# Optimization experiments

Measured on AMD Instinct MI355X. Metric: run time of the kernel, lower is better.

Reference implementation:

```python
import jax, jax.numpy as jnp
import numpy as np

N = 100_000      # nodes
E = 1_600_000    # edges
F_IN = 32        # node features
F_E = 8          # edge features
H = 64           # hidden channels
L = 2            # GAT layers
NEG_SLOPE = 0.2


def setup_inputs() -> dict:
    key = jax.random.key(0)
    ks = jax.random.split(key, 20)
    s = 0.05
    return {
        "x": jax.random.normal(ks[0], (N, F_IN), jnp.float32),
        "edge_index": jax.random.randint(ks[1], (2, E), 0, N, jnp.int64),
        "edge_attr": jax.random.normal(ks[2], (E, F_E), jnp.float32),
        # node encoder
        "enc_w": jax.random.normal(ks[3], (F_IN, H), jnp.float32) * s,
        "enc_b": jnp.zeros((H,), jnp.float32),
        # GAT layers (stacked over L)
        "gat_w": jax.random.normal(ks[4], (L, H, H), jnp.float32) * s,
        "att_src": jax.random.normal(ks[5], (L, H), jnp.float32) * s,
        "att_dst": jax.random.normal(ks[6], (L, H), jnp.float32) * s,
        "edge_w": jax.random.normal(ks[7], (L, F_E, H), jnp.float32) * s,
        "att_edge": jax.random.normal(ks[8], (L, H), jnp.float32) * s,
        "gat_b": jnp.zeros((L, H), jnp.float32),
        # link predictor MLP
        "lp_w1": jax.random.normal(ks[9], (2 * H, H), jnp.float32) * s,
        "lp_b1": jnp.zeros((H,), jnp.float32),
        "lp_w2": jax.random.normal(ks[10], (H, 1), jnp.float32) * s,
        "lp_b2": jnp.zeros((1,), jnp.float32),
    }


def _gat_conv(h, src, dst, eattr, W, a_src, a_dst, We, a_edge, b):
    """PyG GATConv, heads=1, self-loops already appended to src/dst/eattr."""
    xp = h @ W                                   # [N, H]
    alpha = (
        (xp @ a_src)[src]                        # [E']
        + (xp @ a_dst)[dst]
        + (eattr @ We) @ a_edge
    )
    alpha = jnp.where(alpha > 0, alpha, NEG_SLOPE * alpha)  # leaky_relu
    # segment softmax over destination node
    m = jax.ops.segment_max(alpha, dst, num_segments=N)
    ex = jnp.exp(alpha - m[dst])
    denom = jax.ops.segment_sum(ex, dst, num_segments=N)
    w = ex / (denom[dst] + 1e-16)                # [E']
    out = jax.ops.segment_sum(w[:, None] * xp[src], dst, num_segments=N)
    return out + b


def reference(x, edge_index, edge_attr, enc_w, enc_b, gat_w, att_src, att_dst,
              edge_w, att_edge, gat_b, lp_w1, lp_b1, lp_w2, lp_b2):
    src, dst = edge_index[0], edge_index[1]
    # add self-loops (PyG GATConv default), edge_attr filled with mean
    loop = jnp.arange(N, dtype=src.dtype)
    src_sl = jnp.concatenate([src, loop])
    dst_sl = jnp.concatenate([dst, loop])
    eattr_sl = jnp.concatenate(
        [edge_attr, jnp.broadcast_to(edge_attr.mean(0), (N, F_E))], axis=0)

    h = x @ enc_w + enc_b                        # node encoder [N, H]
    for l in range(L):
        h = jax.nn.relu(_gat_conv(h, src_sl, dst_sl, eattr_sl,
                                  gat_w[l], att_src[l], att_dst[l],
                                  edge_w[l], att_edge[l], gat_b[l]))
    # decode: gather src/dst embeddings, concat, MLP, sigmoid
    ee = jnp.concatenate([h[src], h[dst]], axis=-1)   # [E, 2H]
    logits = jax.nn.relu(ee @ lp_w1 + lp_b1) @ lp_w2 + lp_b2
    return jax.nn.sigmoid(logits).squeeze(-1)         # [E]
```

## Files before the change

kernel.cpp:

```cpp
#include <hip/hip_runtime.h>
#include <hip/hip_bf16.h>
#include <math.h>

#define N_NODES 100000
#define N_EDGES 1600000
#define F_INN   32
#define F_EE    8
#define HD      64
#define E_SL    (N_EDGES + N_NODES)
#define NEG_SLOPE 0.2f
#define NPB 32

#define NBKT 250
#define BKT_W (N_NODES / NBKT)
#define BKT_CAP 7200
#define ME_UNR 10
#define ME_CHUNK (256 * ME_UNR)
#define ME_BLOCKS (N_EDGES / ME_CHUNK)
#define PART_CH (ME_BLOCKS * 4)
#define SB_THREADS 512
#define SEL_CAP (BKT_CAP + BKT_W)

__device__ __forceinline__ float waveReduceSum(float v) {
#pragma unroll
    for (int off = 32; off > 0; off >>= 1) v += __shfl_down(v, off, 64);
    return v;
}
__device__ __forceinline__ float bf_lo(uint u) { return __uint_as_float(u << 16); }
__device__ __forceinline__ float bf_hi(uint u) { return __uint_as_float(u & 0xffff0000u); }
__device__ __forceinline__ uint pack_bf2(float a, float b) {
    __hip_bfloat16 ha = __float2bfloat16(a), hb = __float2bfloat16(b);
    unsigned short ua, ub;
    __builtin_memcpy(&ua, &ha, 2); __builtin_memcpy(&ub, &hb, 2);
    return (uint)ua | ((uint)ub << 16);
}

__global__ void k_init_small(const float* __restrict__ edge_w, const float* __restrict__ att_edge,
                             float* __restrict__ we_vec) {
    int t = threadIdx.x;
    if (t < 16) {
        int l = t >> 3, k = t & 7;
        const float* We = edge_w + l * F_EE * HD + k * HD;
        const float* ae = att_edge + l * HD;
        float s = 0.0f;
#pragma unroll
        for (int j = 0; j < HD; ++j) s += We[j] * ae[j];
        we_vec[l * 8 + k] = s;
    }
}

__global__ __launch_bounds__(256) void k_fuse_w(const float* __restrict__ enc_w,
                                                const float* __restrict__ enc_b,
                                                const float* __restrict__ W0,
                                                float* __restrict__ Wc, float* __restrict__ bc) {
    int t = threadIdx.x;
    for (int idx = t; idx < F_INN * HD; idx += 256) {
        int r = idx >> 6, c = idx & 63;
        float s = 0.0f;
#pragma unroll
        for (int k = 0; k < HD; ++k) s += enc_w[r * HD + k] * W0[k * HD + c];
        Wc[idx] = s;
    }
    if (t < HD) {
        float s = 0.0f;
#pragma unroll
        for (int k = 0; k < HD; ++k) s += enc_b[k] * W0[k * HD + t];
        bc[t] = s;
    }
}

__global__ void k_zero(int* __restrict__ bkt_pos) {
    int t = threadIdx.x;
    if (t < NBKT) bkt_pos[t] = 0;
}

__global__ __launch_bounds__(256) void k_mean_edterm(const float* __restrict__ eattr,
                                                     const int* __restrict__ src,
                                                     const int* __restrict__ dst,
                                                     const float* __restrict__ we_vec,
                                                     float* __restrict__ partials,
                                                     int* __restrict__ bkt,
                                                     int* __restrict__ bkt_pos) {
    __shared__ float sw[16];
    __shared__ int hist[NBKT];
    __shared__ int lstart[256];
    __shared__ int gstart[NBKT];
    __shared__ int recs[ME_CHUNK * 4];
    int t = threadIdx.x;
    if (t < 16) sw[t] = we_vec[t];
    if (t < NBKT) hist[t] = 0;
    __syncthreads();
    float p[8];
#pragma unroll
    for (int k = 0; k < 8; ++k) p[k] = 0.0f;
    int e0 = blockIdx.x * ME_CHUNK;
    int rs[ME_UNR]; uint rp[ME_UNR]; int rb[ME_UNR];
#pragma unroll
    for (int u = 0; u < ME_UNR; ++u) {
        int e = e0 + u * 256 + t;
        const float4* row = (const float4*)(eattr + (size_t)e * F_EE);
        float4 r0 = row[0], r1 = row[1];
        p[0] += r0.x; p[1] += r0.y; p[2] += r0.z; p[3] += r0.w;
        p[4] += r1.x; p[5] += r1.y; p[6] += r1.z; p[7] += r1.w;
        float ed0 = r0.x * sw[0] + r0.y * sw[1] + r0.z * sw[2] + r0.w * sw[3]
                  + r1.x * sw[4] + r1.y * sw[5] + r1.z * sw[6] + r1.w * sw[7];
        float ed1 = r0.x * sw[8] + r0.y * sw[9] + r0.z * sw[10] + r0.w * sw[11]
                  + r1.x * sw[12] + r1.y * sw[13] + r1.z * sw[14] + r1.w * sw[15];
        rs[u] = src[e];
        rp[u] = pack_bf2(ed0, ed1);
        int d = dst[e];
        int b = d / BKT_W;
        rb[u] = (b << 16) | (d - b * BKT_W);
        atomicAdd(&hist[b], 1);
    }
    __syncthreads();
    lstart[t] = (t < NBKT) ? hist[t] : 0;
    __syncthreads();
    for (int off = 1; off < 256; off <<= 1) {
        int x = (t >= off) ? lstart[t - off] : 0;
        __syncthreads();
        lstart[t] += x;
        __syncthreads();
    }
    if (t < NBKT) {
        int v = hist[t];
        gstart[t] = atomicAdd(&bkt_pos[t], v);
        lstart[t] -= v;
        hist[t] = 0;
    }
    __syncthreads();
#pragma unroll
    for (int u = 0; u < ME_UNR; ++u) {
        int b = rb[u] >> 16, dl = rb[u] & 0xFFFF;
        int l = atomicAdd(&hist[b], 1);
        int e = e0 + u * 256 + t;
        ((int4*)recs)[lstart[b] + l] = make_int4(rs[u], (int)rp[u], e, dl);
    }
    __syncthreads();
    int w = t >> 6, lane = t & 63;
    int4* gb4 = (int4*)bkt;
    for (int b = w; b < NBKT; b += 4) {
        int n = hist[b];
        int ls = lstart[b];
        int gs = gstart[b];
        for (int off = lane; off < n; off += 64)
            if (gs + off < BKT_CAP)
                gb4[(size_t)b * BKT_CAP + gs + off] = ((const int4*)recs)[ls + off];
    }
#pragma unroll
    for (int k = 0; k < 8; ++k) p[k] = waveReduceSum(p[k]);
    if ((t & 63) == 0) {
        float* dstp = partials + ((size_t)blockIdx.x * 4 + w) * 8;
#pragma unroll
        for (int k = 0; k < 8; ++k) dstp[k] = p[k];
    }
}

__global__ __launch_bounds__(256) void k_mean_final(const float* __restrict__ partials,
                                                    const float* __restrict__ we_vec,
                                                    uint* __restrict__ ltp) {
    __shared__ float red[256];
    __shared__ float mean8[8];
    __shared__ float lt[2];
    int t = threadIdx.x;
    int k = t & 7;
    int chunk = t >> 3;
    float s = 0.0f;
    for (int i = chunk; i < PART_CH; i += 32) s += partials[(size_t)i * 8 + k];
    red[t] = s;
    __syncthreads();
    if (t < 8) {
        float acc = 0.0f;
#pragma unroll
        for (int c = 0; c < 32; ++c) acc += red[c * 8 + t];
        mean8[t] = acc * (1.0f / N_EDGES);
    }
    __syncthreads();
    if (t < 2) {
        float acc = 0.0f;
#pragma unroll
        for (int kk = 0; kk < 8; ++kk) acc += mean8[kk] * we_vec[t * 8 + kk];
        lt[t] = acc;
    }
    __syncthreads();
    if (t == 0) ltp[0] = pack_bf2(lt[0], lt[1]);
}

__global__ void k_bktscan(const int* __restrict__ bkt_pos, int* __restrict__ bktbase,
                          int* __restrict__ row_ptr) {
    __shared__ int sd[256];
    int t = threadIdx.x;
    int v = (t < NBKT) ? min(bkt_pos[t], BKT_CAP) + BKT_W : 0;
    sd[t] = v;
    __syncthreads();
    for (int off = 1; off < 256; off <<= 1) {
        int x = (t >= off) ? sd[t - off] : 0;
        __syncthreads();
        sd[t] += x;
        __syncthreads();
    }
    if (t < NBKT) bktbase[t] = sd[t] - v;
    if (t == 0) row_ptr[N_NODES] = E_SL;
}

__global__ __launch_bounds__(SB_THREADS) void k_sort_build(const int* __restrict__ bkt_pos,
                                                           const int* __restrict__ bkt,
                                                           const int* __restrict__ bktbase,
                                                           const uint* __restrict__ ltp,
                                                           int2* __restrict__ agg,
                                                           int2* __restrict__ dec,
                                                           int* __restrict__ row_ptr) {
    __shared__ int S[BKT_W];
    __shared__ int cur[BKT_W];
    __shared__ unsigned short sel[SEL_CAP];
    int b = blockIdx.x;
    int t = threadIdx.x;
    int cnt = min(bkt_pos[b], BKT_CAP);
    const int4* bp = (const int4*)bkt + (size_t)b * BKT_CAP;
    if (t < BKT_W) cur[t] = 0;
    __syncthreads();
    for (int i = t; i < cnt; i += SB_THREADS) {
        int4 v = bp[i];
        atomicAdd(&cur[v.w], 1);
    }
    __syncthreads();
    if (t < BKT_W) S[t] = cur[t];
    for (int off = 1; off < BKT_W; off <<= 1) {
        __syncthreads();
        int x = (t >= off && t < BKT_W) ? S[t - off] : 0;
        __syncthreads();
        if (t < BKT_W) S[t] += x;
    }
    __syncthreads();
    int n0 = b * BKT_W;
    int gb = bktbase[b];
    if (t < BKT_W) {
        row_ptr[n0 + t] = gb + (t == 0 ? 0 : S[t - 1]) + t;
        cur[t] = 0;
        sel[S[t] + t] = (unsigned short)(0x8000 | t);
    }
    __syncthreads();
    for (int i = t; i < cnt; i += SB_THREADS) {
        int dl = bp[i].w;
        int r = atomicAdd(&cur[dl], 1);
        int nb = (dl == 0) ? 0 : S[dl - 1];
        sel[nb + dl + r] = (unsigned short)i;
    }
    __syncthreads();
    int total = cnt + BKT_W;
    uint lt = ltp[0];
    for (int p = t; p < total; p += SB_THREADS) {
        unsigned short v = sel[p];
        int2 a, d2;
        if (v & 0x8000) {
            int node = n0 + (v & 0x7fff);
            a = make_int2(node, (int)lt);
            d2 = make_int2(node, -1);
        } else {
            int4 r = bp[v];
            a = make_int2(r.x, r.y);
            d2 = make_int2(r.x, r.z);
        }
        agg[gb + p] = a;
        dec[gb + p] = d2;
    }
}

__global__ __launch_bounds__(256) void k_xp0(const float* __restrict__ x,
                                             const float* __restrict__ Wc,
                                             const float* __restrict__ bc,
                                             const float* __restrict__ a_src,
                                             const float* __restrict__ a_dst,
                                             __hip_bfloat16* __restrict__ xpb,
                                             float* __restrict__ s_src,
                                             float* __restrict__ s_dst) {
    __shared__ float xr[NPB * F_INN];
    int t = threadIdx.x;
    int j = t & 63, wv = t >> 6;
    float4 w[F_INN / 4];
#pragma unroll
    for (int kk = 0; kk < F_INN / 4; ++kk) {
        w[kk].x = Wc[(4 * kk + 0) * HD + j];
        w[kk].y = Wc[(4 * kk + 1) * HD + j];
        w[kk].z = Wc[(4 * kk + 2) * HD + j];
        w[kk].w = Wc[(4 * kk + 3) * HD + j];
    }
    int n0 = blockIdx.x * NPB;
    ((float4*)xr)[t] = ((const float4*)(x + (size_t)n0 * F_INN))[t];
    __syncthreads();
    float asj = a_src[j], adj = a_dst[j], bcj = bc[j];
    for (int n = wv; n < NPB; n += 4) {
        const float4* hx = (const float4*)&xr[n * F_INN];
        float acc = bcj;
#pragma unroll
        for (int kk = 0; kk < F_INN / 4; ++kk) {
            float4 hv = hx[kk];
            acc += hv.x * w[kk].x + hv.y * w[kk].y + hv.z * w[kk].z + hv.w * w[kk].w;
        }
        int node = n0 + n;
        xpb[(size_t)node * HD + j] = __float2bfloat16(acc);
        float ts = waveReduceSum(acc * asj);
        float td = waveReduceSum(acc * adj);
        if (j == 0) { s_src[node] = ts; s_dst[node] = td; }
    }
}

__global__ __launch_bounds__(256) void k_xp(const float* __restrict__ h, const float* __restrict__ W,
                                            const float* __restrict__ a_src, const float* __restrict__ a_dst,
                                            __hip_bfloat16* __restrict__ xpb, float* __restrict__ s_src,
                                            float* __restrict__ s_dst) {
    __shared__ float hr[NPB * HD];
    int t = threadIdx.x;
    int j = t & 63, wv = t >> 6;
    float4 w[HD / 4];
#pragma unroll
    for (int kk = 0; kk < HD / 4; ++kk) {
        w[kk].x = W[(4 * kk + 0) * HD + j];
        w[kk].y = W[(4 * kk + 1) * HD + j];
        w[kk].z = W[(4 * kk + 2) * HD + j];
        w[kk].w = W[(4 * kk + 3) * HD + j];
    }
    int n0 = blockIdx.x * NPB;
#pragma unroll
    for (int i = 0; i < 2; ++i)
        ((float4*)hr)[t + i * 256] = ((const float4*)(h + (size_t)n0 * HD))[t + i * 256];
    __syncthreads();
    float asj = a_src[j], adj = a_dst[j];
    for (int n = wv; n < NPB; n += 4) {
        const float4* hx = (const float4*)&hr[n * HD];
        float acc = 0.0f;
#pragma unroll
        for (int kk = 0; kk < HD / 4; ++kk) {
            float4 hv = hx[kk];
            acc += hv.x * w[kk].x + hv.y * w[kk].y + hv.z * w[kk].z + hv.w * w[kk].w;
        }
        int node = n0 + n;
        xpb[(size_t)node * HD + j] = __float2bfloat16(acc);
        float ts = waveReduceSum(acc * asj);
        float td = waveReduceSum(acc * adj);
        if (j == 0) { s_src[node] = ts; s_dst[node] = td; }
    }
}

template <int LAYER>
__global__ __launch_bounds__(256) void k_aggregate(const int* __restrict__ row_ptr,
                                                   const int2* __restrict__ agg,
                                                   const float* __restrict__ s_src,
                                                   const float* __restrict__ s_dst,
                                                   const uint2* __restrict__ xpr,
                                                   const float* __restrict__ bias,
                                                   float* __restrict__ h) {
    int t = threadIdx.x;
    int node = blockIdx.x * 4 + (t >> 6);
    int lane = t & 63;
    int g = lane >> 4, li = lane & 15;
    int start = row_ptr[node], end = row_ptr[node + 1];
    float sd = s_dst[node];
    float ax = 0.0f, ay = 0.0f, az = 0.0f, aw = 0.0f, den = 0.0f;
    int i = start;
    for (; i + 8 <= end; i += 8) {
        int2 r0 = agg[i + g];
        int2 r1 = agg[i + 4 + g];
        int sp0 = r0.x, sp1 = r1.x;
        uint2 u0 = xpr[(size_t)sp0 * 16 + li];
        uint2 u1 = xpr[(size_t)sp1 * 16 + li];
        float a0 = s_src[sp0] + sd + (LAYER == 0 ? bf_lo((uint)r0.y) : bf_hi((uint)r0.y));
        float a1 = s_src[sp1] + sd + (LAYER == 0 ? bf_lo((uint)r1.y) : bf_hi((uint)r1.y));
        a0 = a0 > 0.0f ? a0 : NEG_SLOPE * a0;
        a1 = a1 > 0.0f ? a1 : NEG_SLOPE * a1;
        float ex0 = __expf(a0), ex1 = __expf(a1);
        den += ex0 + ex1;
        ax += ex0 * bf_lo(u0.x) + ex1 * bf_lo(u1.x);
        ay += ex0 * bf_hi(u0.x) + ex1 * bf_hi(u1.x);
        az += ex0 * bf_lo(u0.y) + ex1 * bf_lo(u1.y);
        aw += ex0 * bf_hi(u0.y) + ex1 * bf_hi(u1.y);
    }
    for (; i < end; i += 4) {
        int idx = i + g;
        bool valid = idx < end;
        int2 r = agg[valid ? idx : end - 1];
        int sp = r.x;
        uint2 u = xpr[(size_t)sp * 16 + li];
        float a = s_src[sp] + sd + (LAYER == 0 ? bf_lo((uint)r.y) : bf_hi((uint)r.y));
        a = a > 0.0f ? a : NEG_SLOPE * a;
        float ex = valid ? __expf(a) : 0.0f;
        den += ex;
        ax += ex * bf_lo(u.x);
        ay += ex * bf_hi(u.x);
        az += ex * bf_lo(u.y);
        aw += ex * bf_hi(u.y);
    }
    den += __shfl_down(den, 32, 64); ax += __shfl_down(ax, 32, 64);
    ay  += __shfl_down(ay, 32, 64); az += __shfl_down(az, 32, 64);
    aw  += __shfl_down(aw, 32, 64);
    den += __shfl_down(den, 16, 64); ax += __shfl_down(ax, 16, 64);
    ay  += __shfl_down(ay, 16, 64); az += __shfl_down(az, 16, 64);
    aw  += __shfl_down(aw, 16, 64);
    if (lane < 16) {
        float inv = 1.0f / (den + 1e-16f);
        float4 b4 = ((const float4*)bias)[li];
        float4 v;
        v.x = fmaxf(ax * inv + b4.x, 0.0f);
        v.y = fmaxf(ay * inv + b4.y, 0.0f);
        v.z = fmaxf(az * inv + b4.z, 0.0f);
        v.w = fmaxf(aw * inv + b4.w, 0.0f);
        ((float4*)(h + (size_t)node * HD))[li] = v;
    }
}

__global__ __launch_bounds__(256) void k_umm(const float* __restrict__ h, const float* __restrict__ w1,
                                             __hip_bfloat16* __restrict__ u1b, float* __restrict__ u2) {
    __shared__ float hr[NPB * HD];
    int t = threadIdx.x;
    int j = t & 63, wv = t >> 6;
    float4 wa[HD / 4], wb[HD / 4];
#pragma unroll
    for (int kk = 0; kk < HD / 4; ++kk) {
        wa[kk].x = w1[(4 * kk + 0) * HD + j];
        wa[kk].y = w1[(4 * kk + 1) * HD + j];
        wa[kk].z = w1[(4 * kk + 2) * HD + j];
        wa[kk].w = w1[(4 * kk + 3) * HD + j];
        wb[kk].x = w1[(HD + 4 * kk + 0) * HD + j];
        wb[kk].y = w1[(HD + 4 * kk + 1) * HD + j];
        wb[kk].z = w1[(HD + 4 * kk + 2) * HD + j];
        wb[kk].w = w1[(HD + 4 * kk + 3) * HD + j];
    }
    int n0 = blockIdx.x * NPB;
#pragma unroll
    for (int i = 0; i < 2; ++i)
        ((float4*)hr)[t + i * 256] = ((const float4*)(h + (size_t)n0 * HD))[t + i * 256];
    __syncthreads();
    for (int n = wv; n < NPB; n += 4) {
        const float4* hx = (const float4*)&hr[n * HD];
        float a1 = 0.0f, a2 = 0.0f;
#pragma unroll
        for (int kk = 0; kk < HD / 4; ++kk) {
            float4 hv = hx[kk];
            a1 += hv.x * wa[kk].x + hv.y * wa[kk].y + hv.z * wa[kk].z + hv.w * wa[kk].w;
            a2 += hv.x * wb[kk].x + hv.y * wb[kk].y + hv.z * wb[kk].z + hv.w * wb[kk].w;
        }
        int node = n0 + n;
        u1b[(size_t)node * HD + j] = __float2bfloat16(a1);
        u2[(size_t)node * HD + j] = a2;
    }
}

__global__ __launch_bounds__(256) void k_decode_csr(const int* __restrict__ row_ptr,
                                                    const int2* __restrict__ dec,
                                                    const uint2* __restrict__ u1r,
                                                    const float* __restrict__ u2,
                                                    const float* __restrict__ b1,
                                                    const float* __restrict__ w2,
                                                    const float* __restrict__ b2,
                                                    float* __restrict__ out) {
    int t = threadIdx.x;
    int node = blockIdx.x * 4 + (t >> 6);
    int lane = t & 63;
    int g = lane >> 4, li = lane & 15;
    float4 c4 = ((const float4*)(u2 + (size_t)node * HD))[li];
    float4 b14 = ((const float4*)b1)[li];
    float4 w4 = ((const float4*)w2)[li];
    c4.x += b14.x; c4.y += b14.y; c4.z += b14.z; c4.w += b14.w;
    float bb = b2[0];
    int start = row_ptr[node], end = row_ptr[node + 1];
    int i = start;
    for (; i + 8 <= end; i += 8) {
        int2 e0 = dec[i + g];
        int2 e1 = dec[i + 4 + g];
        uint2 ua = u1r[(size_t)e0.x * 16 + li];
        uint2 ub = u1r[(size_t)e1.x * 16 + li];
        float p0 = fmaxf(bf_lo(ua.x) + c4.x, 0.0f) * w4.x
                 + fmaxf(bf_hi(ua.x) + c4.y, 0.0f) * w4.y
                 + fmaxf(bf_lo(ua.y) + c4.z, 0.0f) * w4.z
                 + fmaxf(bf_hi(ua.y) + c4.w, 0.0f) * w4.w;
        float p1 = fmaxf(bf_lo(ub.x) + c4.x, 0.0f) * w4.x
                 + fmaxf(bf_hi(ub.x) + c4.y, 0.0f) * w4.y
                 + fmaxf(bf_lo(ub.y) + c4.z, 0.0f) * w4.z
                 + fmaxf(bf_hi(ub.y) + c4.w, 0.0f) * w4.w;
#pragma unroll
        for (int off = 8; off > 0; off >>= 1) {
            p0 += __shfl_down(p0, off, 16);
            p1 += __shfl_down(p1, off, 16);
        }
        if (li == 0) {
            if (e0.y >= 0) out[e0.y] = 1.0f / (1.0f + __expf(-(p0 + bb)));
            if (e1.y >= 0) out[e1.y] = 1.0f / (1.0f + __expf(-(p1 + bb)));
        }
    }
    for (; i < end; i += 4) {
        int idx = i + g;
        bool valid = idx < end;
        int2 e = dec[valid ? idx : end - 1];
        uint2 u = u1r[(size_t)e.x * 16 + li];
        float p = fmaxf(bf_lo(u.x) + c4.x, 0.0f) * w4.x
                + fmaxf(bf_hi(u.x) + c4.y, 0.0f) * w4.y
                + fmaxf(bf_lo(u.y) + c4.z, 0.0f) * w4.z
                + fmaxf(bf_hi(u.y) + c4.w, 0.0f) * w4.w;
#pragma unroll
        for (int off = 8; off > 0; off >>= 1) p += __shfl_down(p, off, 16);
        if (li == 0 && valid && e.y >= 0)
            out[e.y] = 1.0f / (1.0f + __expf(-(p + bb)));
    }
}

extern "C" void kernel_launch(void* const* d_in, const int* in_sizes, int n_in,
                              void* d_out, int out_size, void* d_ws, size_t ws_size,
                              hipStream_t stream) {
    const float* x        = (const float*)d_in[0];
    const int*   eidx     = (const int*)d_in[1];
    const float* eattr    = (const float*)d_in[2];
    const float* enc_w    = (const float*)d_in[3];
    const float* enc_b    = (const float*)d_in[4];
    const float* gat_w    = (const float*)d_in[5];
    const float* att_src  = (const float*)d_in[6];
    const float* att_dst  = (const float*)d_in[7];
    const float* edge_w   = (const float*)d_in[8];
    const float* att_edge = (const float*)d_in[9];
    const float* gat_b    = (const float*)d_in[10];
    const float* lp_w1    = (const float*)d_in[11];
    const float* lp_b1    = (const float*)d_in[12];
    const float* lp_w2    = (const float*)d_in[13];
    const float* lp_b2    = (const float*)d_in[14];
    float* out = (float*)d_out;

    const int* src = eidx;
    const int* dst = eidx + N_EDGES;

    float* ws = (float*)d_ws;
    float*  h       = ws;
    int*    bkt     = (int*)h;
    __hip_bfloat16* xpb = (__hip_bfloat16*)(h + (size_t)N_NODES * HD);
    int2*   agg     = (int2*)((char*)xpb + (size_t)N_NODES * HD * 2);
    int2*   dec     = agg + E_SL;
    float*  fsmall    = (float*)(dec + E_SL);
    float*  s_src     = fsmall;
    float*  s_dst     = s_src + N_NODES;
    float*  partials  = s_dst + N_NODES;
    float*  we_vec    = partials + PART_CH * 8;
    uint*   ltp       = (uint*)(we_vec + 16);
    float*  Wc        = (float*)(ltp + 1);
    float*  bc        = Wc + F_INN * HD;
    int*    row_ptr   = (int*)(bc + HD);
    int*    bkt_pos   = row_ptr + N_NODES + 1;
    int*    bktbase   = bkt_pos + NBKT;

    const int NB_AGG  = N_NODES / 4;
    const int NB_DENSE = N_NODES / NPB;

    k_init_small<<<1, 64, 0, stream>>>(edge_w, att_edge, we_vec);
    k_fuse_w<<<1, 256, 0, stream>>>(enc_w, enc_b, gat_w, Wc, bc);
    k_zero<<<1, 256, 0, stream>>>(bkt_pos);
    k_mean_edterm<<<ME_BLOCKS, 256, 0, stream>>>(eattr, src, dst, we_vec,
                                                 partials, bkt, bkt_pos);
    k_mean_final<<<1, 256, 0, stream>>>(partials, we_vec, ltp);

    k_bktscan<<<1, 256, 0, stream>>>(bkt_pos, bktbase, row_ptr);
    k_sort_build<<<NBKT, SB_THREADS, 0, stream>>>(bkt_pos, bkt, bktbase, ltp,
                                                  agg, dec, row_ptr);

    k_xp0<<<NB_DENSE, 256, 0, stream>>>(x, Wc, bc, att_src, att_dst, xpb, s_src, s_dst);
    k_aggregate<0><<<NB_AGG, 256, 0, stream>>>(row_ptr, agg, s_src, s_dst,
                                               (const uint2*)xpb, gat_b, h);
    k_xp<<<NB_DENSE, 256, 0, stream>>>(h, gat_w + HD * HD, att_src + HD, att_dst + HD,
                                       xpb, s_src, s_dst);
    k_aggregate<1><<<NB_AGG, 256, 0, stream>>>(row_ptr, agg, s_src, s_dst,
                                               (const uint2*)xpb, gat_b + HD, h);

    k_umm<<<NB_DENSE, 256, 0, stream>>>(h, lp_w1, xpb, h);
    k_decode_csr<<<NB_AGG, 256, 0, stream>>>(row_ptr, dec, (const uint2*)xpb, h,
                                             lp_b1, lp_w2, lp_b2, out);
}
```

Before: 468.3 us.

## Decode edges in original order and compact bucket records to 8 bytes

Replaces the CSR-ordered decode, which needed a separate dec array of (src, edge id), with a per-edge decode that reads src/dst directly and gathers both endpoint projections in bf16. Bucket records shrink from int4 to uint2 by packing the local destination index into the upper bits of src. The second projection is now stored in bf16 with the bias pre-added, and it reuses the agg buffer. This removes the dec array writes and shrinks sort-traffic bytes. In exchange, decode loses locality on the destination side and adds a second random gather, plus some bf16 rounding of u2.

```diff
diff --git a/kernel.cpp b/kernel.cpp
--- a/kernel.cpp
+++ b/kernel.cpp
@@ -79,13 +79,13 @@
                                                      const int* __restrict__ dst,
                                                      const float* __restrict__ we_vec,
                                                      float* __restrict__ partials,
-                                                     int* __restrict__ bkt,
+                                                     uint* __restrict__ bkt,
                                                      int* __restrict__ bkt_pos) {
     __shared__ float sw[16];
     __shared__ int hist[NBKT];
     __shared__ int lstart[256];
     __shared__ int gstart[NBKT];
-    __shared__ int recs[ME_CHUNK * 4];
+    __shared__ uint recs[ME_CHUNK * 2];
     int t = threadIdx.x;
     if (t < 16) sw[t] = we_vec[t];
     if (t < NBKT) hist[t] = 0;
@@ -133,19 +133,18 @@
     for (int u = 0; u < ME_UNR; ++u) {
         int b = rb[u] >> 16, dl = rb[u] & 0xFFFF;
         int l = atomicAdd(&hist[b], 1);
-        int e = e0 + u * 256 + t;
-        ((int4*)recs)[lstart[b] + l] = make_int4(rs[u], (int)rp[u], e, dl);
+        ((uint2*)recs)[lstart[b] + l] = make_uint2((uint)rs[u] | ((uint)dl << 17), rp[u]);
     }
     __syncthreads();
     int w = t >> 6, lane = t & 63;
-    int4* gb4 = (int4*)bkt;
+    uint2* gb2 = (uint2*)bkt;
     for (int b = w; b < NBKT; b += 4) {
         int n = hist[b];
         int ls = lstart[b];
         int gs = gstart[b];
         for (int off = lane; off < n; off += 64)
             if (gs + off < BKT_CAP)
-                gb4[(size_t)b * BKT_CAP + gs + off] = ((const int4*)recs)[ls + off];
+                gb2[(size_t)b * BKT_CAP + gs + off] = ((const uint2*)recs)[ls + off];
     }
 #pragma unroll
     for (int k = 0; k < 8; ++k) p[k] = waveReduceSum(p[k]);
@@ -204,11 +203,10 @@
 }
 
 __global__ __launch_bounds__(SB_THREADS) void k_sort_build(const int* __restrict__ bkt_pos,
-                                                           const int* __restrict__ bkt,
+                                                           const uint* __restrict__ bkt,
                                                            const int* __restrict__ bktbase,
                                                            const uint* __restrict__ ltp,
                                                            int2* __restrict__ agg,
-                                                           int2* __restrict__ dec,
                                                            int* __restrict__ row_ptr) {
     __shared__ int S[BKT_W];
     __shared__ int cur[BKT_W];
@@ -216,12 +214,12 @@
     int b = blockIdx.x;
     int t = threadIdx.x;
     int cnt = min(bkt_pos[b], BKT_CAP);
-    const int4* bp = (const int4*)bkt + (size_t)b * BKT_CAP;
+    const uint2* bp = (const uint2*)bkt + (size_t)b * BKT_CAP;
     if (t < BKT_W) cur[t] = 0;
     __syncthreads();
     for (int i = t; i < cnt; i += SB_THREADS) {
-        int4 v = bp[i];
-        atomicAdd(&cur[v.w], 1);
+        uint2 v = bp[i];
+        atomicAdd(&cur[v.x >> 17], 1);
     }
     __syncthreads();
     if (t < BKT_W) S[t] = cur[t];
@@ -241,7 +239,7 @@
     }
     __syncthreads();
     for (int i = t; i < cnt; i += SB_THREADS) {
-        int dl = bp[i].w;
+        int dl = (int)(bp[i].x >> 17);
         int r = atomicAdd(&cur[dl], 1);
         int nb = (dl == 0) ? 0 : S[dl - 1];
         sel[nb + dl + r] = (unsigned short)i;
@@ -251,18 +249,14 @@
     uint lt = ltp[0];
     for (int p = t; p < total; p += SB_THREADS) {
         unsigned short v = sel[p];
-        int2 a, d2;
+        int2 a;
         if (v & 0x8000) {
-            int node = n0 + (v & 0x7fff);
-            a = make_int2(node, (int)lt);
-            d2 = make_int2(node, -1);
+            a = make_int2(n0 + (v & 0x7fff), (int)lt);
         } else {
-            int4 r = bp[v];
-            a = make_int2(r.x, r.y);
-            d2 = make_int2(r.x, r.z);
+            uint2 r = bp[v];
+            a = make_int2((int)(r.x & 0x1FFFFu), (int)r.y);
         }
         agg[gb + p] = a;
-        dec[gb + p] = d2;
     }
 }
 
@@ -409,7 +403,9 @@
 }
 
 __global__ __launch_bounds__(256) void k_umm(const float* __restrict__ h, const float* __restrict__ w1,
-                                             __hip_bfloat16* __restrict__ u1b, float* __restrict__ u2) {
+                                             const float* __restrict__ b1,
+                                             __hip_bfloat16* __restrict__ u1b,
+                                             __hip_bfloat16* __restrict__ u2b) {
     __shared__ float hr[NPB * HD];
     int t = threadIdx.x;
     int j = t & 63, wv = t >> 6;
@@ -425,6 +421,7 @@
         wb[kk].z = w1[(HD + 4 * kk + 2) * HD + j];
         wb[kk].w = w1[(HD + 4 * kk + 3) * HD + j];
     }
+    float b1j = b1[j];
     int n0 = blockIdx.x * NPB;
 #pragma unroll
     for (int i = 0; i < 2; ++i)
@@ -441,65 +438,48 @@
         }
         int node = n0 + n;
         u1b[(size_t)node * HD + j] = __float2bfloat16(a1);
-        u2[(size_t)node * HD + j] = a2;
-    }
-}
-
-__global__ __launch_bounds__(256) void k_decode_csr(const int* __restrict__ row_ptr,
-                                                    const int2* __restrict__ dec,
-                                                    const uint2* __restrict__ u1r,
-                                                    const float* __restrict__ u2,
-                                                    const float* __restrict__ b1,
-                                                    const float* __restrict__ w2,
-                                                    const float* __restrict__ b2,
-                                                    float* __restrict__ out) {
-    int t = threadIdx.x;
-    int node = blockIdx.x * 4 + (t >> 6);
-    int lane = t & 63;
-    int g = lane >> 4, li = lane & 15;
-    float4 c4 = ((const float4*)(u2 + (size_t)node * HD))[li];
-    float4 b14 = ((const float4*)b1)[li];
+        u2b[(size_t)node * HD + j] = __float2bfloat16(a2 + b1j);
+    }
+}
+
+__global__ __launch_bounds__(256) void k_decode_edge(const int* __restrict__ src,
+                                                     const int* __restrict__ dst,
+                                                     const uint2* __restrict__ u1r,
+                                                     const uint2* __restrict__ u2r,
+                                                     const float* __restrict__ w2,
+                                                     const float* __restrict__ b2,
+                                                     float* __restrict__ out) {
+    __shared__ int sld[64];
+    int t = threadIdx.x;
+    int e0 = blockIdx.x * 32;
+    if (t < 32) sld[t] = src[e0 + t];
+    else if (t < 64) sld[t] = dst[e0 + t - 32];
+    __syncthreads();
+    int g = t >> 4, li = t & 15;
     float4 w4 = ((const float4*)w2)[li];
-    c4.x += b14.x; c4.y += b14.y; c4.z += b14.z; c4.w += b14.w;
     float bb = b2[0];
-    int start = row_ptr[node], end = row_ptr[node + 1];
-    int i = start;
-    for (; i + 8 <= end; i += 8) {
-        int2 e0 = dec[i + g];
-        int2 e1 = dec[i + 4 + g];
-        uint2 ua = u1r[(size_t)e0.x * 16 + li];
-        uint2 ub = u1r[(size_t)e1.x * 16 + li];
-        float p0 = fmaxf(bf_lo(ua.x) + c4.x, 0.0f) * w4.x
-                 + fmaxf(bf_hi(ua.x) + c4.y, 0.0f) * w4.y
-                 + fmaxf(bf_lo(ua.y) + c4.z, 0.0f) * w4.z
-                 + fmaxf(bf_hi(ua.y) + c4.w, 0.0f) * w4.w;
-        float p1 = fmaxf(bf_lo(ub.x) + c4.x, 0.0f) * w4.x
-                 + fmaxf(bf_hi(ub.x) + c4.y, 0.0f) * w4.y
-                 + fmaxf(bf_lo(ub.y) + c4.z, 0.0f) * w4.z
-                 + fmaxf(bf_hi(ub.y) + c4.w, 0.0f) * w4.w;
-#pragma unroll
-        for (int off = 8; off > 0; off >>= 1) {
-            p0 += __shfl_down(p0, off, 16);
-            p1 += __shfl_down(p1, off, 16);
-        }
-        if (li == 0) {
-            if (e0.y >= 0) out[e0.y] = 1.0f / (1.0f + __expf(-(p0 + bb)));
-            if (e1.y >= 0) out[e1.y] = 1.0f / (1.0f + __expf(-(p1 + bb)));
-        }
-    }
-    for (; i < end; i += 4) {
-        int idx = i + g;
-        bool valid = idx < end;
-        int2 e = dec[valid ? idx : end - 1];
-        uint2 u = u1r[(size_t)e.x * 16 + li];
-        float p = fmaxf(bf_lo(u.x) + c4.x, 0.0f) * w4.x
-                + fmaxf(bf_hi(u.x) + c4.y, 0.0f) * w4.y
-                + fmaxf(bf_lo(u.y) + c4.z, 0.0f) * w4.z
-                + fmaxf(bf_hi(u.y) + c4.w, 0.0f) * w4.w;
-#pragma unroll
-        for (int off = 8; off > 0; off >>= 1) p += __shfl_down(p, off, 16);
-        if (li == 0 && valid && e.y >= 0)
-            out[e.y] = 1.0f / (1.0f + __expf(-(p + bb)));
+    int sa = sld[g],      da = sld[32 + g];
+    int sb = sld[16 + g], db = sld[48 + g];
+    uint2 a1 = u1r[(size_t)sa * 16 + li];
+    uint2 a2 = u2r[(size_t)da * 16 + li];
+    uint2 bq1 = u1r[(size_t)sb * 16 + li];
+    uint2 bq2 = u2r[(size_t)db * 16 + li];
+    float p0 = fmaxf(bf_lo(a1.x) + bf_lo(a2.x), 0.0f) * w4.x
+             + fmaxf(bf_hi(a1.x) + bf_hi(a2.x), 0.0f) * w4.y
+             + fmaxf(bf_lo(a1.y) + bf_lo(a2.y), 0.0f) * w4.z
+             + fmaxf(bf_hi(a1.y) + bf_hi(a2.y), 0.0f) * w4.w;
+    float p1 = fmaxf(bf_lo(bq1.x) + bf_lo(bq2.x), 0.0f) * w4.x
+             + fmaxf(bf_hi(bq1.x) + bf_hi(bq2.x), 0.0f) * w4.y
+             + fmaxf(bf_lo(bq1.y) + bf_lo(bq2.y), 0.0f) * w4.z
+             + fmaxf(bf_hi(bq1.y) + bf_hi(bq2.y), 0.0f) * w4.w;
+#pragma unroll
+    for (int off = 8; off > 0; off >>= 1) {
+        p0 += __shfl_down(p0, off, 16);
+        p1 += __shfl_down(p1, off, 16);
+    }
+    if (li == 0) {
+        out[e0 + g]      = 1.0f / (1.0f + __expf(-(p0 + bb)));
+        out[e0 + 16 + g] = 1.0f / (1.0f + __expf(-(p1 + bb)));
     }
 }
 
@@ -528,11 +508,10 @@
 
     float* ws = (float*)d_ws;
     float*  h       = ws;
-    int*    bkt     = (int*)h;
+    uint*   bkt     = (uint*)h;
     __hip_bfloat16* xpb = (__hip_bfloat16*)(h + (size_t)N_NODES * HD);
     int2*   agg     = (int2*)((char*)xpb + (size_t)N_NODES * HD * 2);
-    int2*   dec     = agg + E_SL;
-    float*  fsmall    = (float*)(dec + E_SL);
+    float*  fsmall    = (float*)(agg + E_SL);
     float*  s_src     = fsmall;
     float*  s_dst     = s_src + N_NODES;
     float*  partials  = s_dst + N_NODES;
@@ -546,6 +525,7 @@
 
     const int NB_AGG  = N_NODES / 4;
     const int NB_DENSE = N_NODES / NPB;
+    const int NB_DEC  = N_EDGES / 32;
 
     k_init_small<<<1, 64, 0, stream>>>(edge_w, att_edge, we_vec);
     k_fuse_w<<<1, 256, 0, stream>>>(enc_w, enc_b, gat_w, Wc, bc);
@@ -556,7 +536,7 @@
 
     k_bktscan<<<1, 256, 0, stream>>>(bkt_pos, bktbase, row_ptr);
     k_sort_build<<<NBKT, SB_THREADS, 0, stream>>>(bkt_pos, bkt, bktbase, ltp,
-                                                  agg, dec, row_ptr);
+                                                  agg, row_ptr);
 
     k_xp0<<<NB_DENSE, 256, 0, stream>>>(x, Wc, bc, att_src, att_dst, xpb, s_src, s_dst);
     k_aggregate<0><<<NB_AGG, 256, 0, stream>>>(row_ptr, agg, s_src, s_dst,
@@ -566,7 +546,8 @@
     k_aggregate<1><<<NB_AGG, 256, 0, stream>>>(row_ptr, agg, s_src, s_dst,
                                                (const uint2*)xpb, gat_b + HD, h);
 
-    k_umm<<<NB_DENSE, 256, 0, stream>>>(h, lp_w1, xpb, h);
-    k_decode_csr<<<NB_AGG, 256, 0, stream>>>(row_ptr, dec, (const uint2*)xpb, h,
-                                             lp_b1, lp_w2, lp_b2, out);
-}
+    k_umm<<<NB_DENSE, 256, 0, stream>>>(h, lp_w1, lp_b1, xpb,
+                                        (__hip_bfloat16*)agg);
+    k_decode_edge<<<NB_DEC, 256, 0, stream>>>(src, dst, (const uint2*)xpb,
+                                              (const uint2*)agg, lp_w2, lp_b2, out);
+}
```

Result: no change. 461.0 us (-1.5%).
